# Kernel optimization log

Hardware: AMD Instinct MI355X
Metric: run time of the kernel (lower is better)

Reference implementation:

```python
import jax, jax.numpy as jnp
import numpy as np

B, T, N, F_IN, F_OUT = 2, 8, 8192, 128, 32

def setup_inputs() -> dict:
    key = jax.random.key(0)
    k1, k2, k3, k4 = jax.random.split(key, 4)
    inp = jax.random.normal(k1, (B, T, N, F_IN), dtype=jnp.float32)
    adj = jax.random.randint(k2, (N, N), 0, 2, dtype=jnp.int32)
    # xavier_uniform with gain=1.414 ~ std = gain*sqrt(2/(fan_in+fan_out)); gaussian approx
    w_std = 1.414 * np.sqrt(2.0 / (F_IN + F_OUT))
    a_std = 1.414 * np.sqrt(2.0 / (2 * F_OUT + N))
    W = jax.random.normal(k3, (F_IN, F_OUT), dtype=jnp.float32) * w_std
    a = jax.random.normal(k4, (2 * F_OUT, N), dtype=jnp.float32) * a_std
    return {"inp": inp, "adj": adj, "W": W, "a": a}

def reference(inp, adj, W, a):
    # h: [B,T,N,out]
    h = jnp.einsum('btni,io->btno', inp, W)
    out = W.shape[1]
    # mask[j,i] = 1 if j is a neighbor of i (original: torch.where(adj[:, i] > 0))
    mask = (adj > 0).astype(h.dtype)
    # neighbor sum per destination node i: [B,T,N,out]
    nbr = jnp.einsum('ji,btjo->btio', mask, h)
    a1 = a[:out].T   # [N, out], per-node first half of attention vector
    a2 = a[out:].T   # [N, out], per-node second half
    # scalar score per (b,t,i); broadcast across j in the original attention matrix.
    # no-neighbor case coincides since nbr is zero there.
    s = jnp.einsum('btno,no->btn', h, a1) + jnp.einsum('btno,no->btn', nbr, a2)
    # h_prime[b,t,i,:] = s[b,t,i] * sum_j h[b,t,j,:]  (attention row is constant)
    h_prime = s[..., None] * jnp.sum(h, axis=2, keepdims=True)
    return jax.nn.relu(h_prime)
```

## Files before the change

kernel.cpp:

```cpp
#include <hip/hip_runtime.h>

#define BT 16
#define NN 8192
#define FIN 128
#define FOUT 32
#define NB 512
#define SPLITK 4
#define KSPAN (NN / SPLITK)
#define BKK 64
#define PADK 72

typedef __attribute__((ext_vector_type(8))) short short8;
typedef __attribute__((ext_vector_type(4))) float float4v;

__device__ __forceinline__ float bf2f(unsigned short u) {
    unsigned v = ((unsigned)u) << 16;
    float f;
    __builtin_memcpy(&f, &v, 4);
    return f;
}
__device__ __forceinline__ unsigned short f2bf(float f) {
    unsigned u;
    __builtin_memcpy(&u, &f, 4);
    u += 0x7FFFu + ((u >> 16) & 1u);
    return (unsigned short)(u >> 16);
}

__device__ __forceinline__ void load_lds16(const unsigned short* g, unsigned short* l) {
    __builtin_amdgcn_global_load_lds((const __attribute__((address_space(1))) void*)g,
                                     (__attribute__((address_space(3))) void*)l, 16, 0, 0);
}

__global__ void sniff_dtype(const unsigned* __restrict__ Wraw, unsigned* __restrict__ flag,
                            float* __restrict__ sumh) {
    int lane = threadIdx.x;
    unsigned u = Wraw[lane];
    float f = bf2f((unsigned short)(u & 0xFFFFu));
    float af = fabsf(f);
    bool plaus = (af > 1e-5f) && (af < 1e3f);
    unsigned long long msk = __ballot(plaus);
    if (lane == 0) flag[0] = (__popcll(msk) >= 32) ? 1u : 0u;
#pragma unroll
    for (int r = 0; r < 8; ++r) sumh[lane + 64 * r] = 0.f;
}

__launch_bounds__(256)
__global__ void k01(const int* __restrict__ adj, unsigned* __restrict__ P,
                    const void* __restrict__ inp_raw, const void* __restrict__ W_raw,
                    unsigned short* __restrict__ Ht, float* __restrict__ sumh,
                    float4* __restrict__ s2v, const unsigned* __restrict__ flagp) {
    __shared__ __align__(16) unsigned short Wt[32 * 136];
    int bid = blockIdx.x;
    const int tid = threadIdx.x;

    if (bid < 128) {
        float4 z; z.x = z.y = z.z = z.w = 0.f;
        s2v[bid * 256 + tid] = z;
        return;
    }
    bid -= 128;
    if (bid < 1024) {
        const int i = (bid & 31) * 256 + tid;
        const int k0 = (bid >> 5) * 256;
        const int w0 = k0 >> 5;
        unsigned words[8];
#pragma unroll
        for (int wk = 0; wk < 8; ++wk) {
            unsigned wv = 0;
            const int* gp = adj + (size_t)(k0 + wk * 32) * NN + i;
#pragma unroll
            for (int kk = 0; kk < 32; ++kk)
                wv |= (gp[(size_t)kk * NN] > 0 ? 1u : 0u) << kk;
            words[wk] = wv;
        }
#pragma unroll
        for (int wk = 0; wk < 8; ++wk)
            P[(size_t)(w0 + wk) * NN + i] = words[wk];
        return;
    }
    bid -= 1024;
    const int bt = bid >> 6;
    const int j0 = (bid & 63) * 128;
    const bool isbf = (*flagp != 0u);

    if (isbf) {
        const unsigned short* Wb = (const unsigned short*)W_raw;
#pragma unroll
        for (int r = 0; r < 16; ++r) {
            int idx = tid + 256 * r, i = idx >> 5, o = idx & 31;
            Wt[o * 136 + i] = Wb[idx];
        }
    } else {
        const float* Wf = (const float*)W_raw;
#pragma unroll
        for (int r = 0; r < 16; ++r) {
            int idx = tid + 256 * r, i = idx >> 5, o = idx & 31;
            Wt[o * 136 + i] = f2bf(Wf[idx]);
        }
    }
    __syncthreads();

    const int lane = tid & 63, w = tid >> 6;
    const int m = lane & 15, q = lane >> 4;
    const int mt = (w & 1) * 16;
    const int nt = (w >> 1) * 64;

    float4v acc[4];
#pragma unroll
    for (int c = 0; c < 4; ++c) { float4v z = {0.f, 0.f, 0.f, 0.f}; acc[c] = z; }

#pragma unroll
    for (int kstep = 0; kstep < 4; ++kstep) {
        short8 af = *(const short8*)&Wt[(mt + m) * 136 + kstep * 32 + q * 8];
#pragma unroll
        for (int c = 0; c < 4; ++c) {
            int j = j0 + nt + c * 16 + m;
            short8 bfrag;
            if (isbf) {
                bfrag = *(const short8*)((const unsigned short*)inp_raw +
                        ((size_t)bt * NN + j) * FIN + kstep * 32 + q * 8);
            } else {
                const float* fp = (const float*)inp_raw + ((size_t)bt * NN + j) * FIN + kstep * 32 + q * 8;
                float4 f0 = *(const float4*)fp;
                float4 f1 = *(const float4*)(fp + 4);
                union { unsigned short u[8]; short8 v; } t;
                t.u[0] = f2bf(f0.x); t.u[1] = f2bf(f0.y); t.u[2] = f2bf(f0.z); t.u[3] = f2bf(f0.w);
                t.u[4] = f2bf(f1.x); t.u[5] = f2bf(f1.y); t.u[6] = f2bf(f1.z); t.u[7] = f2bf(f1.w);
                bfrag = t.v;
            }
            acc[c] = __builtin_amdgcn_mfma_f32_16x16x32_bf16(af, bfrag, acc[c], 0, 0, 0);
        }
    }

#pragma unroll
    for (int c = 0; c < 4; ++c) {
#pragma unroll
        for (int e = 0; e < 4; ++e) {
            int o = mt + q * 4 + e;
            int j = j0 + nt + c * 16 + m;
            Ht[(size_t)(bt * FOUT + o) * NN + j] = f2bf(acc[c][e]);
        }
    }
#pragma unroll
    for (int e = 0; e < 4; ++e) {
        float s = acc[0][e] + acc[1][e] + acc[2][e] + acc[3][e];
        s += __shfl_xor(s, 1); s += __shfl_xor(s, 2);
        s += __shfl_xor(s, 4); s += __shfl_xor(s, 8);
        if (m == 0) atomicAdd(&sumh[bt * FOUT + mt + q * 4 + e], s);
    }
}

__launch_bounds__(256, 4)
__global__ void k2_gemm(const unsigned* __restrict__ P, const unsigned short* __restrict__ Ht,
                        const void* __restrict__ a_raw, float* __restrict__ s2,
                        const unsigned* __restrict__ flagp) {
    __shared__ __align__(16) unsigned short As[128 * PADK];
    __shared__ __align__(16) unsigned short Bs[128 * 64];
    const int tid = threadIdx.x;
    const int n0 = blockIdx.x * 128;
    const int i0 = blockIdx.y * 128;
    const int z = blockIdx.z;
    const int lane = tid & 63, w = tid >> 6;
    const int m = lane & 15, q = lane >> 4;
    const int wm = (w >> 1) * 64, wn = (w & 1) * 64;

    int boff[4];
#pragma unroll
    for (int c = 0; c < 4; ++c) {
        int u = (w * 4 + c) * 64 + lane;
        int n = u >> 3;
        int kbs = (u & 7) ^ (n & 7);
        boff[c] = (n0 + n) * NN + kbs * 8;
    }

    float4v acc[4][4];
#pragma unroll
    for (int r = 0; r < 4; ++r)
#pragma unroll
        for (int c = 0; c < 4; ++c) { float4v zz = {0.f, 0.f, 0.f, 0.f}; acc[r][c] = zz; }

    const int si = tid & 127;
    const int kh = tid >> 7;
    const unsigned* Prow = P + (size_t)((z * KSPAN) >> 5) * NN + i0 + si + (size_t)kh * NN;

    for (int ks0 = 0; ks0 < KSPAN; ks0 += BKK) {
        const int k0 = z * KSPAN + ks0;
        __syncthreads();
#pragma unroll
        for (int c = 0; c < 4; ++c)
            load_lds16(Ht + boff[c] + k0, &Bs[(w * 4 + c) * 512]);
        {
            unsigned word = Prow[(size_t)(ks0 >> 5) * NN];
            unsigned pk[16];
#pragma unroll
            for (int p = 0; p < 16; ++p) {
                unsigned b0 = (word >> (2 * p)) & 1u;
                unsigned b1 = (word >> (2 * p + 1)) & 1u;
                pk[p] = (b0 ? 0x3F80u : 0u) | (b1 ? 0x3F800000u : 0u);
            }
            unsigned short* dst = &As[si * PADK + kh * 32];
#pragma unroll
            for (int qq = 0; qq < 4; ++qq) {
                int4 t;
                t.x = (int)pk[qq * 4 + 0]; t.y = (int)pk[qq * 4 + 1];
                t.z = (int)pk[qq * 4 + 2]; t.w = (int)pk[qq * 4 + 3];
                *(int4*)(dst + qq * 8) = t;
            }
        }
        __syncthreads();
#pragma unroll
        for (int ks = 0; ks < 2; ++ks) {
            short8 af[4], bfr[4];
#pragma unroll
            for (int r = 0; r < 4; ++r)
                af[r] = *(const short8*)&As[(wm + r * 16 + m) * PADK + ks * 32 + q * 8];
#pragma unroll
            for (int c = 0; c < 4; ++c) {
                int row = wn + c * 16 + m;
                int kbs = (ks * 4 + q) ^ (m & 7);
                bfr[c] = *(const short8*)&Bs[row * 64 + kbs * 8];
            }
#pragma unroll
            for (int r = 0; r < 4; ++r)
#pragma unroll
                for (int c = 0; c < 4; ++c)
                    acc[r][c] = __builtin_amdgcn_mfma_f32_16x16x32_bf16(af[r], bfr[c], acc[r][c], 0, 0, 0);
        }
    }

    const bool isbf = (*flagp != 0u);
    const int btA = (n0 + wn) >> 5;
#pragma unroll
    for (int r = 0; r < 4; ++r) {
#pragma unroll
        for (int e = 0; e < 4; ++e) {
            int gi = i0 + wm + r * 16 + q * 4 + e;
            float a2m, a2m16;
            if (isbf) {
                const unsigned short* ab = (const unsigned short*)a_raw;
                a2m   = bf2f(ab[(size_t)(FOUT + m) * NN + gi]);
                a2m16 = bf2f(ab[(size_t)(FOUT + 16 + m) * NN + gi]);
            } else {
                const float* afp = (const float*)a_raw;
                a2m   = afp[(size_t)(FOUT + m) * NN + gi];
                a2m16 = afp[(size_t)(FOUT + 16 + m) * NN + gi];
            }
            float sA = acc[r][0][e] * a2m + acc[r][1][e] * a2m16;
            float sB = acc[r][2][e] * a2m + acc[r][3][e] * a2m16;
            sA += __shfl_xor(sA, 1); sA += __shfl_xor(sA, 2);
            sA += __shfl_xor(sA, 4); sA += __shfl_xor(sA, 8);
            sB += __shfl_xor(sB, 1); sB += __shfl_xor(sB, 2);
            sB += __shfl_xor(sB, 4); sB += __shfl_xor(sB, 8);
            if (m == 0) {
                atomicAdd(&s2[(size_t)btA * NN + gi], sA);
                atomicAdd(&s2[(size_t)(btA + 1) * NN + gi], sB);
            }
        }
    }
}

__launch_bounds__(256)
__global__ void k3_out(const unsigned short* __restrict__ Ht, const float* __restrict__ s2,
                       const float* __restrict__ sumh, const void* __restrict__ a_raw,
                       void* __restrict__ out_raw, const unsigned* __restrict__ flagp) {
    const int i = blockIdx.x * 256 + threadIdx.x;
    const int bt = blockIdx.y;
    const bool isbf = (*flagp != 0u);

    float s = s2[(size_t)bt * NN + i];
    if (isbf) {
        const unsigned short* ab = (const unsigned short*)a_raw;
#pragma unroll
        for (int o = 0; o < 32; ++o) {
            float h = bf2f(Ht[(size_t)(bt * FOUT + o) * NN + i]);
            s += h * bf2f(ab[(size_t)o * NN + i]);
        }
    } else {
        const float* afp = (const float*)a_raw;
#pragma unroll
        for (int o = 0; o < 32; ++o) {
            float h = bf2f(Ht[(size_t)(bt * FOUT + o) * NN + i]);
            s += h * afp[(size_t)o * NN + i];
        }
    }

    float ov[32];
#pragma unroll
    for (int o = 0; o < 32; ++o) ov[o] = fmaxf(s * sumh[bt * FOUT + o], 0.f);

    size_t ob = ((size_t)bt * NN + i) * FOUT;
    if (isbf) {
        unsigned short* o16 = (unsigned short*)out_raw + ob;
#pragma unroll
        for (int c = 0; c < 8; ++c) {
            ushort4 p;
            p.x = f2bf(ov[c * 4 + 0]); p.y = f2bf(ov[c * 4 + 1]);
            p.z = f2bf(ov[c * 4 + 2]); p.w = f2bf(ov[c * 4 + 3]);
            *(ushort4*)(o16 + c * 4) = p;
        }
    } else {
        float* of = (float*)out_raw + ob;
#pragma unroll
        for (int c = 0; c < 8; ++c) {
            float4 v;
            v.x = ov[c * 4 + 0]; v.y = ov[c * 4 + 1]; v.z = ov[c * 4 + 2]; v.w = ov[c * 4 + 3];
            *(float4*)(of + c * 4) = v;
        }
    }
}

extern "C" void kernel_launch(void* const* d_in, const int* in_sizes, int n_in,
                              void* d_out, int out_size, void* d_ws, size_t ws_size,
                              hipStream_t stream) {
    const void* inp = d_in[0];
    const int* adj = (const int*)d_in[1];
    const void* W = d_in[2];
    const void* a = d_in[3];

    char* ws = (char*)d_ws;
    unsigned short* Ht = (unsigned short*)ws;
    unsigned* P = (unsigned*)(ws + 8388608);
    unsigned* flag = (unsigned*)(ws + 16777216);
    float* s2 = (float*)(ws + 16781312);
    float* sumh = (float*)(ws + 16781312 + 524288);

    sniff_dtype<<<1, 64, 0, stream>>>((const unsigned*)W, flag, sumh);
    k01<<<2176, 256, 0, stream>>>(adj, P, inp, W, Ht, sumh, (float4*)s2, flag);
    k2_gemm<<<dim3(NB / 128, NN / 128, SPLITK), 256, 0, stream>>>(P, Ht, a, s2, flag);
    k3_out<<<dim3(NN / 256, BT), 256, 0, stream>>>(Ht, s2, sumh, a, d_out, flag);
}
```

Before: 502.2 us.

## Fuse adjacency bit-packing into GEMM, read adj directly with full-N tiles

Drops the separate pass that packs the int32 adjacency into bitmasks and has the GEMM kernel read adj columns directly, converting them to bf16 0/1 tiles in LDS with one tile of register prefetch. The GEMM block now covers all 512 output columns (B·T·F_OUT) for 64 destination nodes, so each adj element is read once, and blocks are mapped to XCDs by split-k index for L2 locality. This removes the packed-P write and read round trip and the extra kernel work. In exchange, each block streams 4-byte adj values, a 4x larger read than the packed bits, and uses a larger Bs LDS buffer with 512 threads, which may lower occupancy.

```diff
diff --git a/kernel.cpp b/kernel.cpp
--- a/kernel.cpp
+++ b/kernel.cpp
@@ -45,10 +45,9 @@
 }
 
 __launch_bounds__(256)
-__global__ void k01(const int* __restrict__ adj, unsigned* __restrict__ P,
-                    const void* __restrict__ inp_raw, const void* __restrict__ W_raw,
-                    unsigned short* __restrict__ Ht, float* __restrict__ sumh,
-                    float4* __restrict__ s2v, const unsigned* __restrict__ flagp) {
+__global__ void k1(const void* __restrict__ inp_raw, const void* __restrict__ W_raw,
+                   unsigned short* __restrict__ Ht, float* __restrict__ sumh,
+                   float4* __restrict__ s2v, const unsigned* __restrict__ flagp) {
     __shared__ __align__(16) unsigned short Wt[32 * 136];
     int bid = blockIdx.x;
     const int tid = threadIdx.x;
@@ -59,26 +58,6 @@
         return;
     }
     bid -= 128;
-    if (bid < 1024) {
-        const int i = (bid & 31) * 256 + tid;
-        const int k0 = (bid >> 5) * 256;
-        const int w0 = k0 >> 5;
-        unsigned words[8];
-#pragma unroll
-        for (int wk = 0; wk < 8; ++wk) {
-            unsigned wv = 0;
-            const int* gp = adj + (size_t)(k0 + wk * 32) * NN + i;
-#pragma unroll
-            for (int kk = 0; kk < 32; ++kk)
-                wv |= (gp[(size_t)kk * NN] > 0 ? 1u : 0u) << kk;
-            words[wk] = wv;
-        }
-#pragma unroll
-        for (int wk = 0; wk < 8; ++wk)
-            P[(size_t)(w0 + wk) * NN + i] = words[wk];
-        return;
-    }
-    bid -= 1024;
     const int bt = bid >> 6;
     const int j0 = (bid & 63) * 128;
     const bool isbf = (*flagp != 0u);
@@ -150,28 +129,37 @@
     }
 }
 
-__launch_bounds__(256, 4)
-__global__ void k2_gemm(const unsigned* __restrict__ P, const unsigned short* __restrict__ Ht,
-                        const void* __restrict__ a_raw, float* __restrict__ s2,
-                        const unsigned* __restrict__ flagp) {
-    __shared__ __align__(16) unsigned short As[128 * PADK];
-    __shared__ __align__(16) unsigned short Bs[128 * 64];
+__launch_bounds__(512, 4)
+__global__ void k2_fused(const int* __restrict__ adj, const unsigned short* __restrict__ Ht,
+                         const void* __restrict__ a_raw, float* __restrict__ s2,
+                         const unsigned* __restrict__ flagp) {
+    __shared__ __align__(16) unsigned short As[64 * PADK];
+    __shared__ __align__(16) unsigned short Bs[512 * 64];
     const int tid = threadIdx.x;
-    const int n0 = blockIdx.x * 128;
-    const int i0 = blockIdx.y * 128;
-    const int z = blockIdx.z;
-    const int lane = tid & 63, w = tid >> 6;
+    const int lane = tid & 63;
+    const int w = tid >> 6;
     const int m = lane & 15, q = lane >> 4;
-    const int wm = (w >> 1) * 64, wn = (w & 1) * 64;
-
-    int boff[4];
-#pragma unroll
-    for (int c = 0; c < 4; ++c) {
-        int u = (w * 4 + c) * 64 + lane;
+    const int wn = w * 64;
+
+    const int bid = blockIdx.x;
+    const int xcd = bid & 7;
+    const int z = xcd >> 1;
+    const int ib = (bid >> 3) | ((xcd & 1) << 6);
+    const int i0 = ib * 64;
+    const int zbase = z * KSPAN;
+
+    int boff[8];
+#pragma unroll
+    for (int c = 0; c < 8; ++c) {
+        int u = (w * 8 + c) * 64 + lane;
         int n = u >> 3;
         int kbs = (u & 7) ^ (n & 7);
-        boff[c] = (n0 + n) * NN + kbs * 8;
-    }
+        boff[c] = n * NN + kbs * 8;
+    }
+
+    const int si = lane;
+    const int kh = w;
+    const int* gcol = adj + (size_t)(zbase + kh * 8) * NN + i0 + si;
 
     float4v acc[4][4];
 #pragma unroll
@@ -179,62 +167,59 @@
 #pragma unroll
         for (int c = 0; c < 4; ++c) { float4v zz = {0.f, 0.f, 0.f, 0.f}; acc[r][c] = zz; }
 
-    const int si = tid & 127;
-    const int kh = tid >> 7;
-    const unsigned* Prow = P + (size_t)((z * KSPAN) >> 5) * NN + i0 + si + (size_t)kh * NN;
+    int av[8];
+#pragma unroll
+    for (int kk = 0; kk < 8; ++kk) av[kk] = gcol[(size_t)kk * NN];
 
     for (int ks0 = 0; ks0 < KSPAN; ks0 += BKK) {
-        const int k0 = z * KSPAN + ks0;
+        const int k0 = zbase + ks0;
         __syncthreads();
 #pragma unroll
-        for (int c = 0; c < 4; ++c)
-            load_lds16(Ht + boff[c] + k0, &Bs[(w * 4 + c) * 512]);
+        for (int c = 0; c < 8; ++c)
+            load_lds16(Ht + boff[c] + k0, &Bs[(w * 8 + c) * 512]);
         {
-            unsigned word = Prow[(size_t)(ks0 >> 5) * NN];
-            unsigned pk[16];
-#pragma unroll
-            for (int p = 0; p < 16; ++p) {
-                unsigned b0 = (word >> (2 * p)) & 1u;
-                unsigned b1 = (word >> (2 * p + 1)) & 1u;
-                pk[p] = (b0 ? 0x3F80u : 0u) | (b1 ? 0x3F800000u : 0u);
-            }
-            unsigned short* dst = &As[si * PADK + kh * 32];
-#pragma unroll
-            for (int qq = 0; qq < 4; ++qq) {
-                int4 t;
-                t.x = (int)pk[qq * 4 + 0]; t.y = (int)pk[qq * 4 + 1];
-                t.z = (int)pk[qq * 4 + 2]; t.w = (int)pk[qq * 4 + 3];
-                *(int4*)(dst + qq * 8) = t;
-            }
+            unsigned d[4];
+#pragma unroll
+            for (int p = 0; p < 4; ++p) {
+                unsigned lo = (av[2 * p]     > 0) ? 0x3F80u     : 0u;
+                unsigned hi = (av[2 * p + 1] > 0) ? 0x3F800000u : 0u;
+                d[p] = lo | hi;
+            }
+            int4 t;
+            t.x = (int)d[0]; t.y = (int)d[1]; t.z = (int)d[2]; t.w = (int)d[3];
+            *(int4*)&As[si * PADK + kh * 8] = t;
+        }
+        if (ks0 + BKK < KSPAN) {
+#pragma unroll
+            for (int kk = 0; kk < 8; ++kk)
+                av[kk] = gcol[(size_t)(ks0 + BKK + kk) * NN];
         }
         __syncthreads();
 #pragma unroll
         for (int ks = 0; ks < 2; ++ks) {
-            short8 af[4], bfr[4];
+            short8 af[4];
 #pragma unroll
             for (int r = 0; r < 4; ++r)
-                af[r] = *(const short8*)&As[(wm + r * 16 + m) * PADK + ks * 32 + q * 8];
+                af[r] = *(const short8*)&As[(r * 16 + m) * PADK + ks * 32 + q * 8];
 #pragma unroll
             for (int c = 0; c < 4; ++c) {
                 int row = wn + c * 16 + m;
                 int kbs = (ks * 4 + q) ^ (m & 7);
-                bfr[c] = *(const short8*)&Bs[row * 64 + kbs * 8];
-            }
-#pragma unroll
-            for (int r = 0; r < 4; ++r)
-#pragma unroll
-                for (int c = 0; c < 4; ++c)
-                    acc[r][c] = __builtin_amdgcn_mfma_f32_16x16x32_bf16(af[r], bfr[c], acc[r][c], 0, 0, 0);
+                short8 bfr = *(const short8*)&Bs[row * 64 + kbs * 8];
+#pragma unroll
+                for (int r = 0; r < 4; ++r)
+                    acc[r][c] = __builtin_amdgcn_mfma_f32_16x16x32_bf16(af[r], bfr, acc[r][c], 0, 0, 0);
+            }
         }
     }
 
     const bool isbf = (*flagp != 0u);
-    const int btA = (n0 + wn) >> 5;
+    const int btA = wn >> 5;
 #pragma unroll
     for (int r = 0; r < 4; ++r) {
 #pragma unroll
         for (int e = 0; e < 4; ++e) {
-            int gi = i0 + wm + r * 16 + q * 4 + e;
+            int gi = i0 + r * 16 + q * 4 + e;
             float a2m, a2m16;
             if (isbf) {
                 const unsigned short* ab = (const unsigned short*)a_raw;
@@ -319,13 +304,12 @@
 
     char* ws = (char*)d_ws;
     unsigned short* Ht = (unsigned short*)ws;
-    unsigned* P = (unsigned*)(ws + 8388608);
-    unsigned* flag = (unsigned*)(ws + 16777216);
-    float* s2 = (float*)(ws + 16781312);
-    float* sumh = (float*)(ws + 16781312 + 524288);
+    unsigned* flag = (unsigned*)(ws + 8388608);
+    float* s2 = (float*)(ws + 8388608 + 4096);
+    float* sumh = (float*)(ws + 8388608 + 4096 + 524288);
 
     sniff_dtype<<<1, 64, 0, stream>>>((const unsigned*)W, flag, sumh);
-    k01<<<2176, 256, 0, stream>>>(adj, P, inp, W, Ht, sumh, (float4*)s2, flag);
-    k2_gemm<<<dim3(NB / 128, NN / 128, SPLITK), 256, 0, stream>>>(P, Ht, a, s2, flag);
+    k1<<<1152, 256, 0, stream>>>(inp, W, Ht, sumh, (float4*)s2, flag);
+    k2_fused<<<512, 512, 0, stream>>>(adj, Ht, a, s2, flag);
     k3_out<<<dim3(NN / 256, BT), 256, 0, stream>>>(Ht, s2, sumh, a, d_out, flag);
 }
```

Result: faster. 467.4 us (-6.9%).
